# Performance work log

Measured on AMD Instinct MI355X. Metric: run time of the kernel, lower is better.

The kernel has to match this reference:

```python
import jax, jax.numpy as jnp
import numpy as np

B, S, D, E = 8, 1024, 2048, 2  # batch, seq, model_dim, num_experts

def setup_inputs() -> dict:
    key = jax.random.key(0)
    k0, k1, k2, k3 = jax.random.split(key, 4)
    x = jax.random.normal(k0, (B, S, D), dtype=jnp.float32)
    wg = jax.random.normal(k1, (D, E), dtype=jnp.float32) * 0.02          # gate projection
    W = jax.random.normal(k2, (E, D, D), dtype=jnp.float32) / np.sqrt(D)  # expert weights [E, in, out]
    b = jax.random.normal(k3, (E, D), dtype=jnp.float32) * 0.02           # expert biases
    return {"x": x, "wg": wg, "W": W, "b": b}

def reference(x, wg, W, b):
    # --- Top1 gate ---
    logits = jnp.einsum('bsd,de->bse', x, wg)          # [B,S,E]
    gates = jax.nn.softmax(logits, axis=-1)
    idx = jnp.argmax(gates, axis=-1)                   # [B,S] top-1 expert per token
    gate_val = jnp.max(gates, axis=-1)                 # [B,S] top-1 gate prob
    # --- Expert GEMMs (dense over the 2 experts, then select == dispatch+combine) ---
    expert_out = jnp.einsum('bsd,edh->ebsh', x, W) + b[:, None, None, :]  # [E,B,S,D]
    onehot = jax.nn.one_hot(idx, E, dtype=x.dtype)     # [B,S,E]
    moe_out = jnp.einsum('bse,ebsh->bsh', onehot, expert_out) * gate_val[..., None]  # [B,S,D]
    # --- einsum('ijk->ij') then log_softmax(dim=1) ---
    y = jnp.sum(moe_out, axis=-1)                      # [B,S]
    return jax.nn.log_softmax(y, axis=1)
```

## Files before the change

### kernel.cpp

```cpp
#include <hip/hip_runtime.h>

#define B_ 8
#define S_ 1024
#define D_ 2048
#define E_ 2
#define NROWS (E_ * D_ + E_)

typedef float f32x4 __attribute__((ext_vector_type(4)));

__device__ inline float wave_reduce_sum(float v) {
    #pragma unroll
    for (int off = 32; off > 0; off >>= 1) v += __shfl_down(v, off, 64);
    return v;
}
__device__ inline float wave_reduce_max(float v) {
    #pragma unroll
    for (int off = 32; off > 0; off >>= 1) v = fmaxf(v, __shfl_down(v, off, 64));
    return v;
}

__global__ __launch_bounds__(256) void reduce_rows_kernel(
        const float* __restrict__ W, const float* __restrict__ bvec,
        float* __restrict__ Wsum, float* __restrict__ bsum) {
    const int wave = threadIdx.x >> 6, lane = threadIdx.x & 63;
    const int row = blockIdx.x * 4 + wave;
    if (row >= NROWS) return;
    const float* src = (row < E_ * D_) ? (W + (size_t)row * D_)
                                       : (bvec + (size_t)(row - E_ * D_) * D_);
    const f32x4* s4 = (const f32x4*)src;
    float s = 0.0f;
    #pragma unroll
    for (int j = 0; j < D_ / 4 / 64; ++j) {
        f32x4 v = __builtin_nontemporal_load(&s4[lane + j * 64]);
        s += (v.x + v.y) + (v.z + v.w);
    }
    s = wave_reduce_sum(s);
    if (lane == 0) {
        if (row < E_ * D_) Wsum[row] = s;
        else               bsum[row - E_ * D_] = s;
    }
}

__global__ __launch_bounds__(256) void token_kernel(
        const float* __restrict__ x, const float* __restrict__ wg,
        const float* __restrict__ Wsum, const float* __restrict__ bsum,
        float* __restrict__ y) {
    const int wave = threadIdx.x >> 6, lane = threadIdx.x & 63;
    const int tok = blockIdx.x * 4 + wave;
    const f32x4* x4  = (const f32x4*)(x + (size_t)tok * D_);
    const f32x4* w0  = (const f32x4*)(Wsum);
    const f32x4* w1  = (const f32x4*)(Wsum + D_);
    const f32x4* wg4 = (const f32x4*)(wg);

    float d0 = 0.0f, d1 = 0.0f, g0 = 0.0f, g1 = 0.0f;
    #pragma unroll
    for (int j = 0; j < D_ / 4 / 64; ++j) {
        const int i = lane + j * 64;
        f32x4 xv = __builtin_nontemporal_load(&x4[i]);
        f32x4 a  = w0[i];
        f32x4 c  = w1[i];
        f32x4 u  = wg4[2 * i];
        f32x4 v  = wg4[2 * i + 1];
        d0 += xv.x * a.x + xv.y * a.y + xv.z * a.z + xv.w * a.w;
        d1 += xv.x * c.x + xv.y * c.y + xv.z * c.z + xv.w * c.w;
        g0 += xv.x * u.x + xv.y * u.z + xv.z * v.x + xv.w * v.z;
        g1 += xv.x * u.y + xv.y * u.w + xv.z * v.y + xv.w * v.w;
    }
    d0 = wave_reduce_sum(d0);
    d1 = wave_reduce_sum(d1);
    g0 = wave_reduce_sum(g0);
    g1 = wave_reduce_sum(g1);

    if (lane == 0) {
        const int idx = (g1 > g0) ? 1 : 0;
        const float diff = idx ? (g0 - g1) : (g1 - g0);
        const float gate = 1.0f / (1.0f + expf(diff));
        const float dot  = idx ? d1 : d0;
        y[tok] = gate * (dot + bsum[idx]);
    }
}

__global__ __launch_bounds__(256) void logsoftmax_kernel(
        const float* __restrict__ y, float* __restrict__ out) {
    const int b = blockIdx.x;
    const f32x4* row4 = (const f32x4*)(y + (size_t)b * S_);
    f32x4 v = row4[threadIdx.x];

    float m = fmaxf(fmaxf(v.x, v.y), fmaxf(v.z, v.w));
    m = wave_reduce_max(m);
    __shared__ float lds[4];
    __shared__ float M_s, L_s;
    const int wave = threadIdx.x >> 6, lane = threadIdx.x & 63;
    if (lane == 0) lds[wave] = m;
    __syncthreads();
    if (threadIdx.x == 0)
        M_s = fmaxf(fmaxf(lds[0], lds[1]), fmaxf(lds[2], lds[3]));
    __syncthreads();
    const float M = M_s;

    float s = expf(v.x - M) + expf(v.y - M) + expf(v.z - M) + expf(v.w - M);
    s = wave_reduce_sum(s);
    __syncthreads();
    if (lane == 0) lds[wave] = s;
    __syncthreads();
    if (threadIdx.x == 0)
        L_s = M + logf(lds[0] + lds[1] + lds[2] + lds[3]);
    __syncthreads();
    const float lse = L_s;

    f32x4 o;
    o.x = v.x - lse; o.y = v.y - lse; o.z = v.z - lse; o.w = v.w - lse;
    ((f32x4*)(out + (size_t)b * S_))[threadIdx.x] = o;
}

extern "C" void kernel_launch(void* const* d_in, const int* in_sizes, int n_in,
                              void* d_out, int out_size, void* d_ws, size_t ws_size,
                              hipStream_t stream) {
    const float* x  = (const float*)d_in[0];
    const float* wg = (const float*)d_in[1];
    const float* W  = (const float*)d_in[2];
    const float* bv = (const float*)d_in[3];
    float* out = (float*)d_out;

    float* ws   = (float*)d_ws;
    float* Wsum = ws;
    float* bsum = ws + E_ * D_;
    float* y    = ws + E_ * D_ + 16;

    reduce_rows_kernel<<<(NROWS + 3) / 4, 256, 0, stream>>>(W, bv, Wsum, bsum);
    token_kernel<<<B_ * S_ / 4, 256, 0, stream>>>(x, wg, Wsum, bsum, y);
    logsoftmax_kernel<<<B_, 256, 0, stream>>>(y, out);
}
```

Baseline: 30.70 us.

## Stage gate and summed expert weights in LDS, process two tokens per wave

The token kernel now copies the summed expert weight vectors and the de-interleaved gate weights into shared memory once per block. Each wave then handles two tokens, so every weight read is reused across both. The goal is to cut repeated L2 traffic for the weight vectors and raise memory-level parallelism on the x stream. In exchange the kernel uses 32 KB of LDS per block, which may limit occupancy, and each block pays a staging cost before its compute starts.

```diff
diff --git a/kernel.cpp b/kernel.cpp
--- a/kernel.cpp
+++ b/kernel.cpp
@@ -45,38 +45,75 @@
         const float* __restrict__ x, const float* __restrict__ wg,
         const float* __restrict__ Wsum, const float* __restrict__ bsum,
         float* __restrict__ y) {
-    const int wave = threadIdx.x >> 6, lane = threadIdx.x & 63;
-    const int tok = blockIdx.x * 4 + wave;
-    const f32x4* x4  = (const f32x4*)(x + (size_t)tok * D_);
-    const f32x4* w0  = (const f32x4*)(Wsum);
-    const f32x4* w1  = (const f32x4*)(Wsum + D_);
-    const f32x4* wg4 = (const f32x4*)(wg);
+    __shared__ float lw0[D_], lw1[D_], lg0[D_], lg1[D_];
+    const int tid = threadIdx.x;
 
-    float d0 = 0.0f, d1 = 0.0f, g0 = 0.0f, g1 = 0.0f;
+    {
+        const f32x4* w0g = (const f32x4*)(Wsum);
+        const f32x4* w1g = (const f32x4*)(Wsum + D_);
+        const f32x4* wgg = (const f32x4*)(wg);
+        f32x4* l0 = (f32x4*)lw0; f32x4* l1 = (f32x4*)lw1;
+        f32x4* g0 = (f32x4*)lg0; f32x4* g1 = (f32x4*)lg1;
+        #pragma unroll
+        for (int i = tid; i < D_ / 4; i += 256) {
+            l0[i] = w0g[i];
+            l1[i] = w1g[i];
+            f32x4 u = wgg[2 * i];
+            f32x4 v = wgg[2 * i + 1];
+            f32x4 a, b;
+            a.x = u.x; a.y = u.z; a.z = v.x; a.w = v.z;
+            b.x = u.y; b.y = u.w; b.z = v.y; b.w = v.w;
+            g0[i] = a;
+            g1[i] = b;
+        }
+    }
+    __syncthreads();
+
+    const int wave = tid >> 6, lane = tid & 63;
+    const int t0 = blockIdx.x * 8 + wave * 2;
+    const int t1 = t0 + 1;
+    const f32x4* xa = (const f32x4*)(x + (size_t)t0 * D_);
+    const f32x4* xb = (const f32x4*)(x + (size_t)t1 * D_);
+    const f32x4* l0 = (const f32x4*)lw0;
+    const f32x4* l1 = (const f32x4*)lw1;
+    const f32x4* c0 = (const f32x4*)lg0;
+    const f32x4* c1 = (const f32x4*)lg1;
+
+    float d0a = 0, d1a = 0, g0a = 0, g1a = 0;
+    float d0b = 0, d1b = 0, g0b = 0, g1b = 0;
     #pragma unroll
     for (int j = 0; j < D_ / 4 / 64; ++j) {
         const int i = lane + j * 64;
-        f32x4 xv = __builtin_nontemporal_load(&x4[i]);
-        f32x4 a  = w0[i];
-        f32x4 c  = w1[i];
-        f32x4 u  = wg4[2 * i];
-        f32x4 v  = wg4[2 * i + 1];
-        d0 += xv.x * a.x + xv.y * a.y + xv.z * a.z + xv.w * a.w;
-        d1 += xv.x * c.x + xv.y * c.y + xv.z * c.z + xv.w * c.w;
-        g0 += xv.x * u.x + xv.y * u.z + xv.z * v.x + xv.w * v.z;
-        g1 += xv.x * u.y + xv.y * u.w + xv.z * v.y + xv.w * v.w;
+        f32x4 x0 = __builtin_nontemporal_load(&xa[i]);
+        f32x4 x1 = __builtin_nontemporal_load(&xb[i]);
+        f32x4 a = l0[i], c = l1[i], u = c0[i], v = c1[i];
+        d0a += x0.x * a.x + x0.y * a.y + x0.z * a.z + x0.w * a.w;
+        d1a += x0.x * c.x + x0.y * c.y + x0.z * c.z + x0.w * c.w;
+        g0a += x0.x * u.x + x0.y * u.y + x0.z * u.z + x0.w * u.w;
+        g1a += x0.x * v.x + x0.y * v.y + x0.z * v.z + x0.w * v.w;
+        d0b += x1.x * a.x + x1.y * a.y + x1.z * a.z + x1.w * a.w;
+        d1b += x1.x * c.x + x1.y * c.y + x1.z * c.z + x1.w * c.w;
+        g0b += x1.x * u.x + x1.y * u.y + x1.z * u.z + x1.w * u.w;
+        g1b += x1.x * v.x + x1.y * v.y + x1.z * v.z + x1.w * v.w;
     }
-    d0 = wave_reduce_sum(d0);
-    d1 = wave_reduce_sum(d1);
-    g0 = wave_reduce_sum(g0);
-    g1 = wave_reduce_sum(g1);
+    d0a = wave_reduce_sum(d0a); d1a = wave_reduce_sum(d1a);
+    g0a = wave_reduce_sum(g0a); g1a = wave_reduce_sum(g1a);
+    d0b = wave_reduce_sum(d0b); d1b = wave_reduce_sum(d1b);
+    g0b = wave_reduce_sum(g0b); g1b = wave_reduce_sum(g1b);
 
     if (lane == 0) {
-        const int idx = (g1 > g0) ? 1 : 0;
-        const float diff = idx ? (g0 - g1) : (g1 - g0);
-        const float gate = 1.0f / (1.0f + expf(diff));
-        const float dot  = idx ? d1 : d0;
-        y[tok] = gate * (dot + bsum[idx]);
+        {
+            const int idx = (g1a > g0a) ? 1 : 0;
+            const float diff = idx ? (g0a - g1a) : (g1a - g0a);
+            const float gate = 1.0f / (1.0f + expf(diff));
+            y[t0] = gate * ((idx ? d1a : d0a) + bsum[idx]);
+        }
+        {
+            const int idx = (g1b > g0b) ? 1 : 0;
+            const float diff = idx ? (g0b - g1b) : (g1b - g0b);
+            const float gate = 1.0f / (1.0f + expf(diff));
+            y[t1] = gate * ((idx ? d1b : d0b) + bsum[idx]);
+        }
     }
 }
 
@@ -128,6 +165,6 @@
     float* y    = ws + E_ * D_ + 16;
 
     reduce_rows_kernel<<<(NROWS + 3) / 4, 256, 0, stream>>>(W, bv, Wsum, bsum);
-    token_kernel<<<B_ * S_ / 4, 256, 0, stream>>>(x, wg, Wsum, bsum, y);
+    token_kernel<<<B_ * S_ / 8, 256, 0, stream>>>(x, wg, Wsum, bsum, y);
     logsoftmax_kernel<<<B_, 256, 0, stream>>>(y, out);
 }
```

Result: faster. 25.73 us (-16.2%).
